# Kernel tuning notes

Measured on AMD Instinct MI355X. Metric: run time of the kernel, lower is better.

Reference implementation:

```python
import jax, jax.numpy as jnp
import numpy as np

DIM = 256
HEADS = 8
HEAD_DIM = 32
WS = 64
MLP = 1024
INNER = HEADS * HEAD_DIM
EPS = 1e-5


def setup_inputs() -> dict:
    key = jax.random.key(0)
    ks = jax.random.split(key, 10)
    B, N = 2, 65536
    s = lambda fan_in: 1.0 / np.sqrt(fan_in)
    return {
        "x": jax.random.normal(ks[0], (B, N, DIM), jnp.float32),
        "w_qkv": jax.random.normal(ks[1], (DIM, 3 * INNER), jnp.float32) * s(DIM),
        "w_out": jax.random.normal(ks[2], (INNER, DIM), jnp.float32) * s(INNER),
        "b_out": jnp.zeros((DIM,), jnp.float32),
        "pos_emb": jax.random.normal(ks[3], (WS, WS), jnp.float32),
        "ln1_g": jnp.ones((DIM,), jnp.float32),
        "ln1_b": jnp.zeros((DIM,), jnp.float32),
        "w1": jax.random.normal(ks[4], (DIM, MLP), jnp.float32) * s(DIM),
        "b1": jnp.zeros((MLP,), jnp.float32),
        "w2": jax.random.normal(ks[5], (MLP, DIM), jnp.float32) * s(MLP),
        "b2": jnp.zeros((DIM,), jnp.float32),
        "ln2_g": jnp.ones((DIM,), jnp.float32),
        "ln2_b": jnp.zeros((DIM,), jnp.float32),
    }


def layernorm(x, g, b):
    mu = jnp.mean(x, axis=-1, keepdims=True)
    var = jnp.var(x, axis=-1, keepdims=True)
    return (x - mu) * jax.lax.rsqrt(var + EPS) * g + b


def window_attn(x, w_qkv, w_out, b_out, pos_emb):
    # shifted window attention (displacement = WS // 2)
    disp = WS // 2
    x = jnp.roll(x, -disp, axis=1)
    b, n, _ = x.shape
    n_w = n // WS
    qkv = x @ w_qkv  # [b, n, 3*inner]
    qkv = qkv.reshape(b, n_w, WS, 3, HEADS, HEAD_DIM)
    q = jnp.transpose(qkv[:, :, :, 0], (0, 3, 1, 2, 4))  # [b, h, n_w, ws, d]
    k = jnp.transpose(qkv[:, :, :, 1], (0, 3, 1, 2, 4))
    v = jnp.transpose(qkv[:, :, :, 2], (0, 3, 1, 2, 4))
    scale = HEAD_DIM ** -0.5
    dots = jnp.einsum("bhwid,bhwjd->bhwij", q, k) * scale + pos_emb
    attn = jax.nn.softmax(dots, axis=-1)
    out = jnp.einsum("bhwij,bhwjd->bhwid", attn, v)
    out = jnp.transpose(out, (0, 2, 3, 1, 4)).reshape(b, n, INNER)
    out = out @ w_out + b_out
    return jnp.roll(out, disp, axis=1)


def reference(x, w_qkv, w_out, b_out, pos_emb, ln1_g, ln1_b, w1, b1, w2, b2, ln2_g, ln2_b):
    # PointSwinBlock: Residual(PreNorm(attn)) then Residual(PreNorm(ffn))
    x = x + window_attn(layernorm(x, ln1_g, ln1_b), w_qkv, w_out, b_out, pos_emb)
    h = layernorm(x, ln2_g, ln2_b)
    h = jax.nn.gelu(h @ w1 + b1, approximate=False) @ w2 + b2
    return x + h
```

## Files before the change

### kernel.cpp

```cpp
#include <hip/hip_runtime.h>
#include <hip/hip_bf16.h>
#include <math.h>
#include <stdint.h>

#define DIM   256
#define NSEQ  65536
#define NTOK  131072
#define HEADS 8
#define HD    32
#define WSZ   64
#define NWIN  2048
#define QKVN  768
#define MLPD  1024
#define LNEPS 1e-5f

typedef __bf16 bf16;
typedef __bf16 bf16x8 __attribute__((ext_vector_type(8)));
typedef __bf16 bf16x4 __attribute__((ext_vector_type(4)));
typedef float  f32x4  __attribute__((ext_vector_type(4)));

__device__ __forceinline__ int roll_row(int r) {
  return (r & 0x10000) | ((r + 32) & 0xFFFF);
}

__device__ __forceinline__ float fast_gelu(float v) {
  const float x2 = v * v;
  const float z2 = v * __builtin_fmaf(x2, 0.07135481630268f, 1.5957691216057308f);
  const float e  = __expf(z2);
  const float r  = __builtin_amdgcn_rcpf(e + 1.0f);
  return __builtin_fmaf(-v, r, v);
}

template<int NY>
__device__ __forceinline__ void grid_swz(int& mBase, int& nBase) {
  const int nwg  = gridDim.x;
  const int lin  = blockIdx.x;
  const int orig = (lin & 7) * (nwg >> 3) + (lin >> 3);
  mBase = (orig / NY) * 128;
  nBase = (orig % NY) * 128;
}

__device__ __forceinline__ void stage16(const bf16* g, bf16* l) {
#if __has_builtin(__builtin_amdgcn_global_load_lds)
  __builtin_amdgcn_global_load_lds((const __attribute__((address_space(1))) void*)g,
                                   (__attribute__((address_space(3))) void*)l, 16, 0, 0);
#else
  int lane = threadIdx.x & 63;
  *(uint4*)((char*)l + lane * 16) = *(const uint4*)g;
#endif
}

template<int K, int LDB, bool ROLL>
__device__ __forceinline__ void gemm_tile(const bf16* __restrict__ A,
                                          const bf16* __restrict__ Bt,
                                          int mBase, int nBase,
                                          bf16* sA, bf16* sB,
                                          f32x4 acc[4][4])
{
  const int tid  = threadIdx.x;
  const int wave = tid >> 6;
  const int lane = tid & 63;
  const int slot = lane & 3;
  const int swz  = (lane >> 3) & 3;
  const int rloc = lane >> 2;
  const int chunk = ((slot ^ swz) * 8);

  int lr0 = mBase + wave * 32 + rloc;
  int lr1 = lr0 + 16;
  int ar0 = ROLL ? roll_row(lr0) : lr0;
  int ar1 = ROLL ? roll_row(lr1) : lr1;
  const bf16* gA0 = A + (size_t)ar0 * K + chunk;
  const bf16* gA1 = A + (size_t)ar1 * K + chunk;
  const bf16* gB0 = Bt + (size_t)(nBase + wave * 32 + rloc) * LDB + chunk;
  const bf16* gB1 = Bt + (size_t)(nBase + wave * 32 + rloc + 16) * LDB + chunk;

  bf16* dA0 = sA + (wave * 32 +  0) * 32;
  bf16* dA1 = sA + (wave * 32 + 16) * 32;
  bf16* dB0 = sB + (wave * 32 +  0) * 32;
  bf16* dB1 = sB + (wave * 32 + 16) * 32;

  const int m0 = (wave & 1) * 64;
  const int n0 = (wave >> 1) * 64;
  const int c    = lane & 15;
  const int quad = lane >> 4;

  int fa[4], fb[4];
#pragma unroll
  for (int t = 0; t < 4; ++t) {
    int rowA = m0 + t * 16 + c;
    fa[t] = rowA * 32 + ((quad ^ ((rowA >> 1) & 3)) * 8);
    int rowB = n0 + t * 16 + c;
    fb[t] = rowB * 32 + ((quad ^ ((rowB >> 1) & 3)) * 8);
  }

  const f32x4 fzero = {0.f, 0.f, 0.f, 0.f};
#pragma unroll
  for (int i = 0; i < 4; ++i)
#pragma unroll
    for (int j = 0; j < 4; ++j) acc[i][j] = fzero;

  stage16(gA0, dA0);
  stage16(gA1, dA1);
  stage16(gB0, dB0);
  stage16(gB1, dB1);
  __syncthreads();

  int cur = 0;
  for (int k0 = 0; k0 < K; k0 += 32) {
    const int nxt = cur ^ 1;
    if (k0 + 32 < K) {
      const int o = nxt * 4096;
      stage16(gA0 + k0 + 32, dA0 + o);
      stage16(gA1 + k0 + 32, dA1 + o);
      stage16(gB0 + k0 + 32, dB0 + o);
      stage16(gB1 + k0 + 32, dB1 + o);
    }
    const int co = cur * 4096;
    bf16x8 afr[4], bfr[4];
#pragma unroll
    for (int t = 0; t < 4; ++t) {
      afr[t] = *(const bf16x8*)(sA + co + fa[t]);
      bfr[t] = *(const bf16x8*)(sB + co + fb[t]);
    }
#pragma unroll
    for (int i = 0; i < 4; ++i)
#pragma unroll
      for (int j = 0; j < 4; ++j)
        acc[i][j] = __builtin_amdgcn_mfma_f32_16x16x32_bf16(afr[i], bfr[j], acc[i][j], 0, 0, 0);
    __syncthreads();
    cur = nxt;
  }
}

__global__ __launch_bounds__(256) void k_prep(const float* __restrict__ wqkv,
                                              const float* __restrict__ wout,
                                              const float* __restrict__ w1,
                                              const float* __restrict__ w2,
                                              const float* __restrict__ pos,
                                              bf16* __restrict__ wqkvT, bf16* __restrict__ woutT,
                                              bf16* __restrict__ w1T, bf16* __restrict__ w2T,
                                              float* __restrict__ posP)
{
  const int total = 768 * 256 + 256 * 256 + 1024 * 256 + 256 * 1024 + 4096;
  for (int i = blockIdx.x * 256 + threadIdx.x; i < total; i += gridDim.x * 256) {
    int j = i;
    if (j < 768 * 256) { int n = j >> 8, k = j & 255; wqkvT[j] = (bf16)wqkv[k * 768 + n]; continue; }
    j -= 768 * 256;
    if (j < 256 * 256) { int n = j >> 8, k = j & 255; woutT[j] = (bf16)wout[k * 256 + n]; continue; }
    j -= 256 * 256;
    if (j < 1024 * 256) { int n = j >> 8, k = j & 255; w1T[j] = (bf16)w1[k * 1024 + n]; continue; }
    j -= 1024 * 256;
    if (j < 256 * 1024) { int n = j >> 10, k = j & 1023; w2T[j] = (bf16)w2[k * 256 + n]; continue; }
    j -= 256 * 1024;
    {
      int lane = j & 63, t = j >> 6;
      int nt = t & 3, r = (t >> 2) & 3, mt = t >> 4;
      int ii = mt * 16 + (lane >> 4) * 4 + r, jj = nt * 16 + (lane & 15);
      posP[j] = pos[ii * 64 + jj];
    }
  }
}

__global__ __launch_bounds__(256) void k_ln(const float* __restrict__ x,
                                            const float* __restrict__ gam,
                                            const float* __restrict__ bet,
                                            bf16* __restrict__ out)
{
  const int wave = threadIdx.x >> 6, lane = threadIdx.x & 63;
  const int token = blockIdx.x * 4 + wave;
  const float4 v = ((const float4*)x)[(size_t)token * 64 + lane];
  float s = v.x + v.y + v.z + v.w;
  float q = v.x * v.x + v.y * v.y + v.z * v.z + v.w * v.w;
#pragma unroll
  for (int off = 32; off; off >>= 1) { s += __shfl_xor(s, off); q += __shfl_xor(q, off); }
  const float mu = s * (1.f / 256.f);
  const float var = q * (1.f / 256.f) - mu * mu;
  const float rs = rsqrtf(var + LNEPS);
  const float4 gv = ((const float4*)gam)[lane];
  const float4 bv = ((const float4*)bet)[lane];
  bf16x4 o;
  o[0] = (bf16)((v.x - mu) * rs * gv.x + bv.x);
  o[1] = (bf16)((v.y - mu) * rs * gv.y + bv.y);
  o[2] = (bf16)((v.z - mu) * rs * gv.z + bv.z);
  o[3] = (bf16)((v.w - mu) * rs * gv.w + bv.w);
  *(bf16x4*)(out + (size_t)token * 256 + lane * 4) = o;
}

__global__ __launch_bounds__(256, 2) void k_gemm_qkv(const bf16* __restrict__ h1,
                                                     const bf16* __restrict__ wqkvT,
                                                     bf16* __restrict__ qkv)
{
  __shared__ __align__(16) bf16 sA[2 * 128 * 32];
  __shared__ __align__(16) bf16 sB[2 * 128 * 32];
  f32x4 acc[4][4];
  int mBase, nBase;
  grid_swz<6>(mBase, nBase);
  gemm_tile<256, 256, true>(h1, wqkvT, mBase, nBase, sA, sB, acc);
  const int lane = threadIdx.x & 63, wave = threadIdx.x >> 6;
  const int c = lane & 15, quad = lane >> 4;
  const int rowBase = mBase + (wave & 1) * 64 + quad * 4;
  const int colBase = nBase + (wave >> 1) * 64 + c;
#pragma unroll
  for (int i = 0; i < 4; ++i)
#pragma unroll
    for (int j = 0; j < 4; ++j)
#pragma unroll
      for (int r = 0; r < 4; ++r)
        qkv[(size_t)(rowBase + i * 16 + r) * QKVN + (colBase + j * 16)] = (bf16)acc[i][j][r];
}

__global__ __launch_bounds__(256, 2) void k_attn(const bf16* __restrict__ qkv,
                                                 const float* __restrict__ posP,
                                                 bf16* __restrict__ attn)
{
  __shared__ __align__(16) bf16 sQ[4][64 * 40];
  __shared__ __align__(16) bf16 sK[4][64 * 40];
  __shared__ __align__(16) bf16 sV[4][32 * 72];
  const int tid = threadIdx.x;
  const int wave = tid >> 6, lane = tid & 63;
  const int gh = blockIdx.y * 4 + wave;
  const int win = blockIdx.x;
  const int c = lane & 15, quad = lane >> 4;
  const size_t base = (size_t)win * 64 * QKVN;

  {
    const int row = lane >> 2;
    const int col = (lane & 3) * 8;
#pragma unroll
    for (int i = 0; i < 4; ++i) {
      int rr = i * 16 + row;
      *(uint4*)(&sQ[wave][rr * 40 + col]) = *(const uint4*)(qkv + base + (size_t)rr * QKVN + gh * 32 + col);
      *(uint4*)(&sK[wave][rr * 40 + col]) = *(const uint4*)(qkv + base + (size_t)rr * QKVN + 256 + gh * 32 + col);
    }
  }
  {
    const int d = lane & 31, jh = lane >> 5;
#pragma unroll
    for (int it = 0; it < 32; ++it) {
      int j = it * 2 + jh;
      sV[wave][d * 72 + j] = qkv[base + (size_t)j * QKVN + 512 + gh * 32 + d];
    }
  }

  const f32x4 fzero = {0.f, 0.f, 0.f, 0.f};
  f32x4 sacc[4][4];
#pragma unroll
  for (int i = 0; i < 4; ++i)
#pragma unroll
    for (int j = 0; j < 4; ++j) sacc[i][j] = fzero;
  bf16x8 qf[4], kf[4];
#pragma unroll
  for (int t = 0; t < 4; ++t) {
    qf[t] = *(const bf16x8*)(&sQ[wave][(t * 16 + c) * 40 + quad * 8]);
    kf[t] = *(const bf16x8*)(&sK[wave][(t * 16 + c) * 40 + quad * 8]);
  }
#pragma unroll
  for (int i = 0; i < 4; ++i)
#pragma unroll
    for (int j = 0; j < 4; ++j)
      sacc[i][j] = __builtin_amdgcn_mfma_f32_16x16x32_bf16(qf[i], kf[j], sacc[i][j], 0, 0, 0);

  const float scale = 0.17677669529663687f;
  float p[4][4][4];
#pragma unroll
  for (int i = 0; i < 4; ++i)
#pragma unroll
    for (int j = 0; j < 4; ++j)
#pragma unroll
      for (int r = 0; r < 4; ++r)
        p[i][j][r] = sacc[i][j][r] * scale + posP[(((i * 4 + r) * 4 + j) << 6) + lane];

  float mx[4][4], rcp[4][4];
#pragma unroll
  for (int i = 0; i < 4; ++i)
#pragma unroll
    for (int r = 0; r < 4; ++r) {
      float m = fmaxf(fmaxf(p[i][0][r], p[i][1][r]), fmaxf(p[i][2][r], p[i][3][r]));
      m = fmaxf(m, __shfl_xor(m, 1)); m = fmaxf(m, __shfl_xor(m, 2));
      m = fmaxf(m, __shfl_xor(m, 4)); m = fmaxf(m, __shfl_xor(m, 8));
      mx[i][r] = m;
    }
#pragma unroll
  for (int i = 0; i < 4; ++i)
#pragma unroll
    for (int r = 0; r < 4; ++r) {
#pragma unroll
      for (int j = 0; j < 4; ++j) p[i][j][r] = __expf(p[i][j][r] - mx[i][r]);
      float t = p[i][0][r] + p[i][1][r] + p[i][2][r] + p[i][3][r];
      t += __shfl_xor(t, 1); t += __shfl_xor(t, 2); t += __shfl_xor(t, 4); t += __shfl_xor(t, 8);
      rcp[i][r] = 1.0f / t;
    }
#pragma unroll
  for (int i = 0; i < 4; ++i)
#pragma unroll
    for (int j = 0; j < 4; ++j)
#pragma unroll
      for (int r = 0; r < 4; ++r) p[i][j][r] *= rcp[i][r];

  f32x4 oacc[4][2];
#pragma unroll
  for (int i = 0; i < 4; ++i) { oacc[i][0] = fzero; oacc[i][1] = fzero; }
#pragma unroll
  for (int half = 0; half < 2; ++half) {
#pragma unroll
    for (int i = 0; i < 4; ++i)
#pragma unroll
      for (int j2 = 0; j2 < 2; ++j2)
#pragma unroll
        for (int r = 0; r < 4; ++r)
          sQ[wave][(i * 16 + quad * 4 + r) * 40 + j2 * 16 + c] = (bf16)p[i][half * 2 + j2][r];
    bf16x8 pf[4], vf[2];
#pragma unroll
    for (int t = 0; t < 4; ++t)
      pf[t] = *(const bf16x8*)(&sQ[wave][(t * 16 + c) * 40 + quad * 8]);
#pragma unroll
    for (int n2 = 0; n2 < 2; ++n2)
      vf[n2] = *(const bf16x8*)(&sV[wave][(n2 * 16 + c) * 72 + half * 32 + quad * 8]);
#pragma unroll
    for (int i = 0; i < 4; ++i)
#pragma unroll
      for (int n2 = 0; n2 < 2; ++n2)
        oacc[i][n2] = __builtin_amdgcn_mfma_f32_16x16x32_bf16(pf[i], vf[n2], oacc[i][n2], 0, 0, 0);
  }

#pragma unroll
  for (int i = 0; i < 4; ++i)
#pragma unroll
    for (int n2 = 0; n2 < 2; ++n2)
#pragma unroll
      for (int r = 0; r < 4; ++r)
        attn[(size_t)(win * 64 + i * 16 + quad * 4 + r) * DIM + gh * 32 + n2 * 16 + c] = (bf16)oacc[i][n2][r];
}

__global__ __launch_bounds__(256, 2) void k_gemm_proj(const bf16* __restrict__ attn,
                                                      const bf16* __restrict__ woutT,
                                                      const float* __restrict__ x,
                                                      const float* __restrict__ b_out,
                                                      float* __restrict__ x2)
{
  __shared__ __align__(16) bf16 sA[2 * 128 * 32];
  __shared__ __align__(16) bf16 sB[2 * 128 * 32];
  f32x4 acc[4][4];
  int mBase, nBase;
  grid_swz<2>(mBase, nBase);
  gemm_tile<256, 256, false>(attn, woutT, mBase, nBase, sA, sB, acc);
  const int lane = threadIdx.x & 63, wave = threadIdx.x >> 6;
  const int c = lane & 15, quad = lane >> 4;
  const int rowBase = mBase + (wave & 1) * 64 + quad * 4;
  const int colBase = nBase + (wave >> 1) * 64 + c;
#pragma unroll
  for (int i = 0; i < 4; ++i)
#pragma unroll
    for (int r = 0; r < 4; ++r) {
      const int rp = rowBase + i * 16 + r;
      const size_t rowoff = (size_t)roll_row(rp) * DIM;
#pragma unroll
      for (int j = 0; j < 4; ++j) {
        const int col = colBase + j * 16;
        x2[rowoff + col] = acc[i][j][r] + b_out[col] + x[rowoff + col];
      }
    }
}

template<int LDC, int NY>
__global__ __launch_bounds__(256, 2) void k_gemm_mlp1(const bf16* __restrict__ h2,
                                                      const bf16* __restrict__ w1Th,
                                                      const float* __restrict__ b1h,
                                                      bf16* __restrict__ g)
{
  __shared__ __align__(16) bf16 sA[2 * 128 * 32];
  __shared__ __align__(16) bf16 sB[2 * 128 * 32];
  f32x4 acc[4][4];
  int mBase, nBase;
  grid_swz<NY>(mBase, nBase);
  gemm_tile<256, 256, false>(h2, w1Th, mBase, nBase, sA, sB, acc);
  const int lane = threadIdx.x & 63, wave = threadIdx.x >> 6;
  const int c = lane & 15, quad = lane >> 4;
  const int rowBase = mBase + (wave & 1) * 64 + quad * 4;
  const int colBase = nBase + (wave >> 1) * 64 + c;
#pragma unroll
  for (int i = 0; i < 4; ++i)
#pragma unroll
    for (int j = 0; j < 4; ++j) {
      const int col = colBase + j * 16;
      const float bb = b1h[col];
#pragma unroll
      for (int r = 0; r < 4; ++r) {
        const float v = acc[i][j][r] + bb;
        g[(size_t)(rowBase + i * 16 + r) * LDC + col] = (bf16)fast_gelu(v);
      }
    }
}

template<int K>
__global__ __launch_bounds__(256, 2) void k_gemm_mlp2(const bf16* __restrict__ g,
                                                      const bf16* __restrict__ w2Th,
                                                      const float* __restrict__ b2,
                                                      float* __restrict__ out,
                                                      int first)
{
  __shared__ __align__(16) bf16 sA[2 * 128 * 32];
  __shared__ __align__(16) bf16 sB[2 * 128 * 32];
  f32x4 acc[4][4];
  int mBase, nBase;
  grid_swz<2>(mBase, nBase);
  gemm_tile<K, 1024, false>(g, w2Th, mBase, nBase, sA, sB, acc);
  const int lane = threadIdx.x & 63, wave = threadIdx.x >> 6;
  const int c = lane & 15, quad = lane >> 4;
  const int rowBase = mBase + (wave & 1) * 64 + quad * 4;
  const int colBase = nBase + (wave >> 1) * 64 + c;
#pragma unroll
  for (int i = 0; i < 4; ++i)
#pragma unroll
    for (int j = 0; j < 4; ++j) {
      const int col = colBase + j * 16;
      const float bb = first ? b2[col] : 0.0f;
#pragma unroll
      for (int r = 0; r < 4; ++r) {
        const size_t off = (size_t)(rowBase + i * 16 + r) * DIM + col;
        out[off] = out[off] + acc[i][j][r] + bb;
      }
    }
}

extern "C" void kernel_launch(void* const* d_in, const int* in_sizes, int n_in,
                              void* d_out, int out_size, void* d_ws, size_t ws_size,
                              hipStream_t stream) {
  const float* x    = (const float*)d_in[0];
  const float* wqkv = (const float*)d_in[1];
  const float* wout = (const float*)d_in[2];
  const float* bo   = (const float*)d_in[3];
  const float* pos  = (const float*)d_in[4];
  const float* l1g  = (const float*)d_in[5];
  const float* l1b  = (const float*)d_in[6];
  const float* w1   = (const float*)d_in[7];
  const float* b1   = (const float*)d_in[8];
  const float* w2   = (const float*)d_in[9];
  const float* b2   = (const float*)d_in[10];
  const float* l2g  = (const float*)d_in[11];
  const float* l2b  = (const float*)d_in[12];
  float* out = (float*)d_out;

  char* ws = (char*)d_ws;
  const size_t WEIGHTS_SZ = (size_t)768 * 256 * 2 + 256 * 256 * 2 + 1024 * 256 * 2
                          + 256 * 1024 * 2 + 4096 * 4;
  const size_t FUSED_NEED = 67108864ull + 268435456ull + WEIGHTS_SZ;
  const bool fused = ws_size >= FUSED_NEED;

  bf16* h1   = (bf16*)ws;
  bf16* qkv  = (bf16*)(ws + 67108864);
  bf16* attn = h1;
  bf16* h2;
  bf16* gbuf;
  char* wp;
  if (fused) {
    h2   = (bf16*)ws;
    gbuf = (bf16*)(ws + 67108864);
    wp   = ws + 67108864 + 268435456;
  } else {
    h2   = qkv;
    gbuf = (bf16*)(ws + 134217728);
    wp   = ws + 268435456;
  }
  bf16* wqkvT = (bf16*)wp;  wp += 768 * 256 * 2;
  bf16* woutT = (bf16*)wp;  wp += 256 * 256 * 2;
  bf16* w1T   = (bf16*)wp;  wp += 1024 * 256 * 2;
  bf16* w2T   = (bf16*)wp;  wp += 256 * 1024 * 2;
  float* posP = (float*)wp;

  k_prep<<<dim3(1024), dim3(256), 0, stream>>>(wqkv, wout, w1, w2, pos, wqkvT, woutT, w1T, w2T, posP);
  k_ln<<<dim3(NTOK / 4), dim3(256), 0, stream>>>(x, l1g, l1b, h1);
  k_gemm_qkv<<<dim3(6144), dim3(256), 0, stream>>>(h1, wqkvT, qkv);
  k_attn<<<dim3(NWIN, 2), dim3(256), 0, stream>>>(qkv, posP, attn);
  k_gemm_proj<<<dim3(2048), dim3(256), 0, stream>>>(attn, woutT, x, bo, out);
  k_ln<<<dim3(NTOK / 4), dim3(256), 0, stream>>>(out, l2g, l2b, h2);
  if (fused) {
    k_gemm_mlp1<1024, 8><<<dim3(8192), dim3(256), 0, stream>>>(h2, w1T, b1, gbuf);
    k_gemm_mlp2<1024><<<dim3(2048), dim3(256), 0, stream>>>(gbuf, w2T, b2, out, 1);
  } else {
    for (int half = 0; half < 2; ++half) {
      k_gemm_mlp1<512, 4><<<dim3(4096), dim3(256), 0, stream>>>(h2, w1T + half * 512 * 256, b1 + half * 512, gbuf);
      k_gemm_mlp2<512><<<dim3(2048), dim3(256), 0, stream>>>(gbuf, w2T + half * 512, b2, out, half == 0 ? 1 : 0);
    }
  }
}
```

Measured before the change: 797.5 us.

## Triple-buffer GEMM LDS staging with partial vmcnt waits and split barriers

Replaces the double-buffered K loop in the shared GEMM tile with a three-stage ring buffer that keeps two async global-to-LDS loads in flight. Each stage waits only for the oldest load using partial vmcnt counts and raw s_barrier instead of a full __syncthreads. Fragment reads are followed by an lgkmcnt wait and a barrier before the MFMAs, so the next overwrite is safe. The goal is to hide more global load latency. The cost is 50% more LDS per block, which could reduce occupancy under the 2-blocks-per-CU launch bound.

```diff
diff --git a/kernel.cpp b/kernel.cpp
--- a/kernel.cpp
+++ b/kernel.cpp
@@ -50,6 +50,28 @@
 #endif
 }
 
+#define TILE_ELEMS 4096
+
+__device__ __forceinline__ void gemm_step(const bf16* sA, const bf16* sB, int co,
+                                          const int fa[4], const int fb[4],
+                                          f32x4 acc[4][4])
+{
+  bf16x8 afr[4], bfr[4];
+#pragma unroll
+  for (int t = 0; t < 4; ++t) {
+    afr[t] = *(const bf16x8*)(sA + co + fa[t]);
+    bfr[t] = *(const bf16x8*)(sB + co + fb[t]);
+  }
+  asm volatile("s_waitcnt lgkmcnt(0)" ::: "memory");
+  __builtin_amdgcn_s_barrier();
+  __builtin_amdgcn_sched_barrier(0);
+#pragma unroll
+  for (int i = 0; i < 4; ++i)
+#pragma unroll
+    for (int j = 0; j < 4; ++j)
+      acc[i][j] = __builtin_amdgcn_mfma_f32_16x16x32_bf16(afr[i], bfr[j], acc[i][j], 0, 0, 0);
+}
+
 template<int K, int LDB, bool ROLL>
 __device__ __forceinline__ void gemm_tile(const bf16* __restrict__ A,
                                           const bf16* __restrict__ Bt,
@@ -99,37 +121,42 @@
 #pragma unroll
     for (int j = 0; j < 4; ++j) acc[i][j] = fzero;
 
+  constexpr int NT = K / 32;
+  static_assert(NT >= 3, "need at least 3 k-chunks");
+
   stage16(gA0, dA0);
   stage16(gA1, dA1);
   stage16(gB0, dB0);
   stage16(gB1, dB1);
-  __syncthreads();
+  stage16(gA0 + 32, dA0 + TILE_ELEMS);
+  stage16(gA1 + 32, dA1 + TILE_ELEMS);
+  stage16(gB0 + 32, dB0 + TILE_ELEMS);
+  stage16(gB1 + 32, dB1 + TILE_ELEMS);
 
   int cur = 0;
-  for (int k0 = 0; k0 < K; k0 += 32) {
-    const int nxt = cur ^ 1;
-    if (k0 + 32 < K) {
-      const int o = nxt * 4096;
-      stage16(gA0 + k0 + 32, dA0 + o);
-      stage16(gA1 + k0 + 32, dA1 + o);
-      stage16(gB0 + k0 + 32, dB0 + o);
-      stage16(gB1 + k0 + 32, dB1 + o);
-    }
-    const int co = cur * 4096;
-    bf16x8 afr[4], bfr[4];
-#pragma unroll
-    for (int t = 0; t < 4; ++t) {
-      afr[t] = *(const bf16x8*)(sA + co + fa[t]);
-      bfr[t] = *(const bf16x8*)(sB + co + fb[t]);
-    }
-#pragma unroll
-    for (int i = 0; i < 4; ++i)
-#pragma unroll
-      for (int j = 0; j < 4; ++j)
-        acc[i][j] = __builtin_amdgcn_mfma_f32_16x16x32_bf16(afr[i], bfr[j], acc[i][j], 0, 0, 0);
-    __syncthreads();
-    cur = nxt;
-  }
+  for (int t = 0; t < NT - 2; ++t) {
+    const int nxt2 = (cur == 0) ? 2 : cur - 1;
+    const int o = nxt2 * TILE_ELEMS;
+    const int k2 = (t + 2) * 32;
+    stage16(gA0 + k2, dA0 + o);
+    stage16(gA1 + k2, dA1 + o);
+    stage16(gB0 + k2, dB0 + o);
+    stage16(gB1 + k2, dB1 + o);
+    asm volatile("s_waitcnt vmcnt(8)" ::: "memory");
+    __builtin_amdgcn_s_barrier();
+    __builtin_amdgcn_sched_barrier(0);
+    gemm_step(sA, sB, cur * TILE_ELEMS, fa, fb, acc);
+    cur = (cur == 2) ? 0 : cur + 1;
+  }
+  asm volatile("s_waitcnt vmcnt(4)" ::: "memory");
+  __builtin_amdgcn_s_barrier();
+  __builtin_amdgcn_sched_barrier(0);
+  gemm_step(sA, sB, cur * TILE_ELEMS, fa, fb, acc);
+  cur = (cur == 2) ? 0 : cur + 1;
+  asm volatile("s_waitcnt vmcnt(0)" ::: "memory");
+  __builtin_amdgcn_s_barrier();
+  __builtin_amdgcn_sched_barrier(0);
+  gemm_step(sA, sB, cur * TILE_ELEMS, fa, fb, acc);
 }
 
 __global__ __launch_bounds__(256) void k_prep(const float* __restrict__ wqkv,
@@ -190,8 +217,8 @@
                                                      const bf16* __restrict__ wqkvT,
                                                      bf16* __restrict__ qkv)
 {
-  __shared__ __align__(16) bf16 sA[2 * 128 * 32];
-  __shared__ __align__(16) bf16 sB[2 * 128 * 32];
+  __shared__ __align__(16) bf16 sA[3 * TILE_ELEMS];
+  __shared__ __align__(16) bf16 sB[3 * TILE_ELEMS];
   f32x4 acc[4][4];
   int mBase, nBase;
   grid_swz<6>(mBase, nBase);
@@ -338,8 +365,8 @@
                                                       const float* __restrict__ b_out,
                                                       float* __restrict__ x2)
 {
-  __shared__ __align__(16) bf16 sA[2 * 128 * 32];
-  __shared__ __align__(16) bf16 sB[2 * 128 * 32];
+  __shared__ __align__(16) bf16 sA[3 * TILE_ELEMS];
+  __shared__ __align__(16) bf16 sB[3 * TILE_ELEMS];
   f32x4 acc[4][4];
   int mBase, nBase;
   grid_swz<2>(mBase, nBase);
@@ -368,8 +395,8 @@
                                                       const float* __restrict__ b1h,
                                                       bf16* __restrict__ g)
 {
-  __shared__ __align__(16) bf16 sA[2 * 128 * 32];
-  __shared__ __align__(16) bf16 sB[2 * 128 * 32];
+  __shared__ __align__(16) bf16 sA[3 * TILE_ELEMS];
+  __shared__ __align__(16) bf16 sB[3 * TILE_ELEMS];
   f32x4 acc[4][4];
   int mBase, nBase;
   grid_swz<NY>(mBase, nBase);
@@ -399,8 +426,8 @@
                                                       float* __restrict__ out,
                                                       int first)
 {
-  __shared__ __align__(16) bf16 sA[2 * 128 * 32];
-  __shared__ __align__(16) bf16 sB[2 * 128 * 32];
+  __shared__ __align__(16) bf16 sA[3 * TILE_ELEMS];
+  __shared__ __align__(16) bf16 sB[3 * TILE_ELEMS];
   f32x4 acc[4][4];
   int mBase, nBase;
   grid_swz<2>(mBase, nBase);
```

Result: no change. 797.1 us (-0.0%).

## Fuse layernorm into QKV GEMM and fuse whole MLP into one kernel

Applied to the files above, without the earlier changes.

Merges LN1 (including the roll) into the QKV projection kernel and LN2, MLP1, GELU and MLP2 into a single per-64-row kernel. The 1024-wide GELU intermediate now stays in LDS in 128-column chunks instead of going through global memory, and the separate normalized-activation buffers are gone. B fragments are read straight from global memory without LDS staging, and the MLP kernel syncs twice per chunk, which may limit MFMA throughput.

```diff
diff --git a/kernel.cpp b/kernel.cpp
--- a/kernel.cpp
+++ b/kernel.cpp
@@ -161,14 +161,9 @@
   }
 }
 
-__global__ __launch_bounds__(256) void k_ln(const float* __restrict__ x,
-                                            const float* __restrict__ gam,
-                                            const float* __restrict__ bet,
-                                            bf16* __restrict__ out)
-{
-  const int wave = threadIdx.x >> 6, lane = threadIdx.x & 63;
-  const int token = blockIdx.x * 4 + wave;
-  const float4 v = ((const float4*)x)[(size_t)token * 64 + lane];
+__device__ __forceinline__ void ln_row_to_lds(const float4 v, const float4 gv, const float4 bv,
+                                              int r, bf16* sA, int lane)
+{
   float s = v.x + v.y + v.z + v.w;
   float q = v.x * v.x + v.y * v.y + v.z * v.z + v.w * v.w;
 #pragma unroll
@@ -176,37 +171,181 @@
   const float mu = s * (1.f / 256.f);
   const float var = q * (1.f / 256.f) - mu * mu;
   const float rs = rsqrtf(var + LNEPS);
-  const float4 gv = ((const float4*)gam)[lane];
-  const float4 bv = ((const float4*)bet)[lane];
   bf16x4 o;
   o[0] = (bf16)((v.x - mu) * rs * gv.x + bv.x);
   o[1] = (bf16)((v.y - mu) * rs * gv.y + bv.y);
   o[2] = (bf16)((v.z - mu) * rs * gv.z + bv.z);
   o[3] = (bf16)((v.w - mu) * rs * gv.w + bv.w);
-  *(bf16x4*)(out + (size_t)token * 256 + lane * 4) = o;
-}
-
-__global__ __launch_bounds__(256, 2) void k_gemm_qkv(const bf16* __restrict__ h1,
-                                                     const bf16* __restrict__ wqkvT,
-                                                     bf16* __restrict__ qkv)
-{
-  __shared__ __align__(16) bf16 sA[2 * 128 * 32];
-  __shared__ __align__(16) bf16 sB[2 * 128 * 32];
-  f32x4 acc[4][4];
-  int mBase, nBase;
-  grid_swz<6>(mBase, nBase);
-  gemm_tile<256, 256, true>(h1, wqkvT, mBase, nBase, sA, sB, acc);
-  const int lane = threadIdx.x & 63, wave = threadIdx.x >> 6;
+  const int q8  = lane >> 3;
+  const int oct = (lane >> 1) & 3;
+  const int w   = (r >> 1) & 3;
+  *(bf16x4*)(sA + q8 * 2048 + r * 32 + ((oct ^ w) * 8) + (lane & 1) * 4) = o;
+}
+
+__global__ __launch_bounds__(512) void k_qkvln(const float* __restrict__ x,
+                                               const float* __restrict__ gam,
+                                               const float* __restrict__ bet,
+                                               const bf16* __restrict__ wqkvT,
+                                               bf16* __restrict__ qkv)
+{
+  __shared__ __align__(16) bf16 sA[8 * 64 * 32];
+  const int tid  = threadIdx.x;
+  const int wave = tid >> 6, lane = tid & 63;
+  const int lin  = blockIdx.x;
+  const int blk  = (lin & 7) * (gridDim.x >> 3) + (lin >> 3);
+  const int m0   = blk * 64;
+
+  {
+    const float4 gv = ((const float4*)gam)[lane];
+    const float4 bv = ((const float4*)bet)[lane];
+#pragma unroll
+    for (int t = 0; t < 8; ++t) {
+      const int r = wave * 8 + t;
+      const float4 v = ((const float4*)x)[(size_t)roll_row(m0 + r) * 64 + lane];
+      ln_row_to_lds(v, gv, bv, r, sA, lane);
+    }
+  }
+  __syncthreads();
+
   const int c = lane & 15, quad = lane >> 4;
-  const int rowBase = mBase + (wave & 1) * 64 + quad * 4;
-  const int colBase = nBase + (wave >> 1) * 64 + c;
-#pragma unroll
-  for (int i = 0; i < 4; ++i)
-#pragma unroll
-    for (int j = 0; j < 4; ++j)
+  int fa[4];
+#pragma unroll
+  for (int t = 0; t < 4; ++t) {
+    int rowA = t * 16 + c;
+    fa[t] = rowA * 32 + ((quad ^ ((rowA >> 1) & 3)) * 8);
+  }
+
+  const f32x4 fzero = {0.f, 0.f, 0.f, 0.f};
+  f32x4 acc[4][6];
+#pragma unroll
+  for (int i = 0; i < 4; ++i)
+#pragma unroll
+    for (int bn = 0; bn < 6; ++bn) acc[i][bn] = fzero;
+
+  const bf16* bp = wqkvT + (size_t)(wave * 96 + c) * 256 + quad * 8;
+#pragma unroll
+  for (int ks = 0; ks < 8; ++ks) {
+    bf16x8 a[4];
+#pragma unroll
+    for (int t = 0; t < 4; ++t) a[t] = *(const bf16x8*)(sA + ks * 2048 + fa[t]);
+    bf16x8 b[6];
+#pragma unroll
+    for (int bn = 0; bn < 6; ++bn) b[bn] = *(const bf16x8*)(bp + (size_t)bn * 16 * 256 + ks * 32);
+#pragma unroll
+    for (int i = 0; i < 4; ++i)
+#pragma unroll
+      for (int bn = 0; bn < 6; ++bn)
+        acc[i][bn] = __builtin_amdgcn_mfma_f32_16x16x32_bf16(a[i], b[bn], acc[i][bn], 0, 0, 0);
+  }
+
+#pragma unroll
+  for (int i = 0; i < 4; ++i)
+#pragma unroll
+    for (int bn = 0; bn < 6; ++bn)
 #pragma unroll
       for (int r = 0; r < 4; ++r)
-        qkv[(size_t)(rowBase + i * 16 + r) * QKVN + (colBase + j * 16)] = (bf16)acc[i][j][r];
+        qkv[(size_t)(m0 + i * 16 + quad * 4 + r) * QKVN + (wave * 96 + bn * 16 + c)] = (bf16)acc[i][bn][r];
+}
+
+__global__ __launch_bounds__(512) void k_mlp(const float* __restrict__ gam,
+                                             const float* __restrict__ bet,
+                                             const bf16* __restrict__ w1T,
+                                             const float* __restrict__ b1,
+                                             const bf16* __restrict__ w2T,
+                                             const float* __restrict__ b2,
+                                             float* out)
+{
+  __shared__ __align__(16) bf16 sA[8 * 64 * 32];
+  __shared__ __align__(16) bf16 sP[4 * 64 * 32];
+  const int tid  = threadIdx.x;
+  const int wave = tid >> 6, lane = tid & 63;
+  const int lin  = blockIdx.x;
+  const int blk  = (lin & 7) * (gridDim.x >> 3) + (lin >> 3);
+  const int m0   = blk * 64;
+
+  {
+    const float4 gv = ((const float4*)gam)[lane];
+    const float4 bv = ((const float4*)bet)[lane];
+#pragma unroll
+    for (int t = 0; t < 8; ++t) {
+      const int r = wave * 8 + t;
+      const float4 v = ((const float4*)out)[(size_t)(m0 + r) * 64 + lane];
+      ln_row_to_lds(v, gv, bv, r, sA, lane);
+    }
+  }
+  __syncthreads();
+
+  const int c = lane & 15, quad = lane >> 4;
+  int fa[4];
+#pragma unroll
+  for (int t = 0; t < 4; ++t) {
+    int rowA = t * 16 + c;
+    fa[t] = rowA * 32 + ((quad ^ ((rowA >> 1) & 3)) * 8);
+  }
+
+  const f32x4 fzero = {0.f, 0.f, 0.f, 0.f};
+  f32x4 acc2[4][2];
+#pragma unroll
+  for (int i = 0; i < 4; ++i) { acc2[i][0] = fzero; acc2[i][1] = fzero; }
+
+  const int nq  = wave >> 1;
+  const int oct = ((wave & 1) << 1) | (c >> 3);
+  const int ncl = c & 7;
+
+  for (int ch = 0; ch < 8; ++ch) {
+    f32x4 acc1[4];
+#pragma unroll
+    for (int i = 0; i < 4; ++i) acc1[i] = fzero;
+    const bf16* bp1 = w1T + (size_t)(ch * 128 + wave * 16 + c) * 256 + quad * 8;
+#pragma unroll
+    for (int ks = 0; ks < 8; ++ks) {
+      bf16x8 a[4];
+#pragma unroll
+      for (int t = 0; t < 4; ++t) a[t] = *(const bf16x8*)(sA + ks * 2048 + fa[t]);
+      const bf16x8 b = *(const bf16x8*)(bp1 + ks * 32);
+#pragma unroll
+      for (int i = 0; i < 4; ++i)
+        acc1[i] = __builtin_amdgcn_mfma_f32_16x16x32_bf16(a[i], b, acc1[i], 0, 0, 0);
+    }
+    __syncthreads();
+    const float bb = b1[ch * 128 + wave * 16 + c];
+#pragma unroll
+    for (int i = 0; i < 4; ++i)
+#pragma unroll
+      for (int r = 0; r < 4; ++r) {
+        const int m = i * 16 + quad * 4 + r;
+        const int w = (m >> 1) & 3;
+        sP[nq * 2048 + m * 32 + ((oct ^ w) * 8) + ncl] = (bf16)fast_gelu(acc1[i][r] + bb);
+      }
+    __syncthreads();
+    const bf16* bp2 = w2T + (size_t)(wave * 32 + c) * 1024 + ch * 128 + quad * 8;
+#pragma unroll
+    for (int ks = 0; ks < 4; ++ks) {
+      bf16x8 pa[4];
+#pragma unroll
+      for (int t = 0; t < 4; ++t) pa[t] = *(const bf16x8*)(sP + ks * 2048 + fa[t]);
+      const bf16x8 b0 = *(const bf16x8*)(bp2 + ks * 32);
+      const bf16x8 b1f = *(const bf16x8*)(bp2 + (size_t)16 * 1024 + ks * 32);
+#pragma unroll
+      for (int i = 0; i < 4; ++i) {
+        acc2[i][0] = __builtin_amdgcn_mfma_f32_16x16x32_bf16(pa[i], b0, acc2[i][0], 0, 0, 0);
+        acc2[i][1] = __builtin_amdgcn_mfma_f32_16x16x32_bf16(pa[i], b1f, acc2[i][1], 0, 0, 0);
+      }
+    }
+  }
+
+#pragma unroll
+  for (int j = 0; j < 2; ++j) {
+    const int col = wave * 32 + j * 16 + c;
+    const float bb2 = b2[col];
+#pragma unroll
+    for (int i = 0; i < 4; ++i)
+#pragma unroll
+      for (int r = 0; r < 4; ++r) {
+        const size_t off = (size_t)(m0 + i * 16 + quad * 4 + r) * DIM + col;
+        out[off] = out[off] + acc2[i][j][r] + bb2;
+      }
+  }
 }
 
 __global__ __launch_bounds__(256, 2) void k_attn(const bf16* __restrict__ qkv,
@@ -338,8 +477,8 @@
                                                       const float* __restrict__ b_out,
                                                       float* __restrict__ x2)
 {
-  __shared__ __align__(16) bf16 sA[2 * 128 * 32];
-  __shared__ __align__(16) bf16 sB[2 * 128 * 32];
+  __shared__ __align__(16) bf16 sA[2 * 4096];
+  __shared__ __align__(16) bf16 sB[2 * 4096];
   f32x4 acc[4][4];
   int mBase, nBase;
   grid_swz<2>(mBase, nBase);
@@ -358,67 +497,6 @@
       for (int j = 0; j < 4; ++j) {
         const int col = colBase + j * 16;
         x2[rowoff + col] = acc[i][j][r] + b_out[col] + x[rowoff + col];
-      }
-    }
-}
-
-template<int LDC, int NY>
-__global__ __launch_bounds__(256, 2) void k_gemm_mlp1(const bf16* __restrict__ h2,
-                                                      const bf16* __restrict__ w1Th,
-                                                      const float* __restrict__ b1h,
-                                                      bf16* __restrict__ g)
-{
-  __shared__ __align__(16) bf16 sA[2 * 128 * 32];
-  __shared__ __align__(16) bf16 sB[2 * 128 * 32];
-  f32x4 acc[4][4];
-  int mBase, nBase;
-  grid_swz<NY>(mBase, nBase);
-  gemm_tile<256, 256, false>(h2, w1Th, mBase, nBase, sA, sB, acc);
-  const int lane = threadIdx.x & 63, wave = threadIdx.x >> 6;
-  const int c = lane & 15, quad = lane >> 4;
-  const int rowBase = mBase + (wave & 1) * 64 + quad * 4;
-  const int colBase = nBase + (wave >> 1) * 64 + c;
-#pragma unroll
-  for (int i = 0; i < 4; ++i)
-#pragma unroll
-    for (int j = 0; j < 4; ++j) {
-      const int col = colBase + j * 16;
-      const float bb = b1h[col];
-#pragma unroll
-      for (int r = 0; r < 4; ++r) {
-        const float v = acc[i][j][r] + bb;
-        g[(size_t)(rowBase + i * 16 + r) * LDC + col] = (bf16)fast_gelu(v);
-      }
-    }
-}
-
-template<int K>
-__global__ __launch_bounds__(256, 2) void k_gemm_mlp2(const bf16* __restrict__ g,
-                                                      const bf16* __restrict__ w2Th,
-                                                      const float* __restrict__ b2,
-                                                      float* __restrict__ out,
-                                                      int first)
-{
-  __shared__ __align__(16) bf16 sA[2 * 128 * 32];
-  __shared__ __align__(16) bf16 sB[2 * 128 * 32];
-  f32x4 acc[4][4];
-  int mBase, nBase;
-  grid_swz<2>(mBase, nBase);
-  gemm_tile<K, 1024, false>(g, w2Th, mBase, nBase, sA, sB, acc);
-  const int lane = threadIdx.x & 63, wave = threadIdx.x >> 6;
-  const int c = lane & 15, quad = lane >> 4;
-  const int rowBase = mBase + (wave & 1) * 64 + quad * 4;
-  const int colBase = nBase + (wave >> 1) * 64 + c;
-#pragma unroll
-  for (int i = 0; i < 4; ++i)
-#pragma unroll
-    for (int j = 0; j < 4; ++j) {
-      const int col = colBase + j * 16;
-      const float bb = first ? b2[col] : 0.0f;
-#pragma unroll
-      for (int r = 0; r < 4; ++r) {
-        const size_t off = (size_t)(rowBase + i * 16 + r) * DIM + col;
-        out[off] = out[off] + acc[i][j][r] + bb;
       }
     }
 }
@@ -442,26 +520,9 @@
   float* out = (float*)d_out;
 
   char* ws = (char*)d_ws;
-  const size_t WEIGHTS_SZ = (size_t)768 * 256 * 2 + 256 * 256 * 2 + 1024 * 256 * 2
-                          + 256 * 1024 * 2 + 4096 * 4;
-  const size_t FUSED_NEED = 67108864ull + 268435456ull + WEIGHTS_SZ;
-  const bool fused = ws_size >= FUSED_NEED;
-
-  bf16* h1   = (bf16*)ws;
-  bf16* qkv  = (bf16*)(ws + 67108864);
-  bf16* attn = h1;
-  bf16* h2;
-  bf16* gbuf;
-  char* wp;
-  if (fused) {
-    h2   = (bf16*)ws;
-    gbuf = (bf16*)(ws + 67108864);
-    wp   = ws + 67108864 + 268435456;
-  } else {
-    h2   = qkv;
-    gbuf = (bf16*)(ws + 134217728);
-    wp   = ws + 268435456;
-  }
+  bf16* qkv  = (bf16*)ws;
+  bf16* attn = (bf16*)(ws + 201326592);
+  char* wp   = ws + 268435456;
   bf16* wqkvT = (bf16*)wp;  wp += 768 * 256 * 2;
   bf16* woutT = (bf16*)wp;  wp += 256 * 256 * 2;
   bf16* w1T   = (bf16*)wp;  wp += 1024 * 256 * 2;
@@ -469,18 +530,8 @@
   float* posP = (float*)wp;
 
   k_prep<<<dim3(1024), dim3(256), 0, stream>>>(wqkv, wout, w1, w2, pos, wqkvT, woutT, w1T, w2T, posP);
-  k_ln<<<dim3(NTOK / 4), dim3(256), 0, stream>>>(x, l1g, l1b, h1);
-  k_gemm_qkv<<<dim3(6144), dim3(256), 0, stream>>>(h1, wqkvT, qkv);
+  k_qkvln<<<dim3(NTOK / 64), dim3(512), 0, stream>>>(x, l1g, l1b, wqkvT, qkv);
   k_attn<<<dim3(NWIN, 2), dim3(256), 0, stream>>>(qkv, posP, attn);
   k_gemm_proj<<<dim3(2048), dim3(256), 0, stream>>>(attn, woutT, x, bo, out);
-  k_ln<<<dim3(NTOK / 4), dim3(256), 0, stream>>>(out, l2g, l2b, h2);
-  if (fused) {
-    k_gemm_mlp1<1024, 8><<<dim3(8192), dim3(256), 0, stream>>>(h2, w1T, b1, gbuf);
-    k_gemm_mlp2<1024><<<dim3(2048), dim3(256), 0, stream>>>(gbuf, w2T, b2, out, 1);
-  } else {
-    for (int half = 0; half < 2; ++half) {
-      k_gemm_mlp1<512, 4><<<dim3(4096), dim3(256), 0, stream>>>(h2, w1T + half * 512 * 256, b1 + half * 512, gbuf);
-      k_gemm_mlp2<512><<<dim3(2048), dim3(256), 0, stream>>>(gbuf, w2T + half * 512, b2, out, half == 0 ? 1 : 0);
-    }
-  }
-}
+  k_mlp<<<dim3(NTOK / 64), dim3(512), 0, stream>>>(l2g, l2b, w1T, b1, w2T, b2, out);
+}
```

Result: slower. 844.8 us (+5.9%).

## Fuse window attention with output projection and residual add into one kernel

Applied to the files above, without the earlier changes.

Window attention and the output projection GEMM now run in one kernel per window. Each block processes all 8 heads for its window, keeps the 64x256 attention output in shared memory, and multiplies it by the projection weight read from global memory. It then adds bias and residual with the roll applied. This removes the bf16 attention intermediate write/read and one launch, and Q/K fragments are now loaded straight from global memory instead of staged through LDS. The cost is a serial loop over heads, half as many blocks, projection weights loaded per block without LDS staging, and more shared memory per block.

```diff
diff --git a/kernel.cpp b/kernel.cpp
--- a/kernel.cpp
+++ b/kernel.cpp
@@ -190,8 +190,8 @@
                                                      const bf16* __restrict__ wqkvT,
                                                      bf16* __restrict__ qkv)
 {
-  __shared__ __align__(16) bf16 sA[2 * 128 * 32];
-  __shared__ __align__(16) bf16 sB[2 * 128 * 32];
+  __shared__ __align__(16) bf16 sA[2 * 4096];
+  __shared__ __align__(16) bf16 sB[2 * 4096];
   f32x4 acc[4][4];
   int mBase, nBase;
   grid_swz<6>(mBase, nBase);
@@ -209,155 +209,159 @@
         qkv[(size_t)(rowBase + i * 16 + r) * QKVN + (colBase + j * 16)] = (bf16)acc[i][j][r];
 }
 
-__global__ __launch_bounds__(256, 2) void k_attn(const bf16* __restrict__ qkv,
-                                                 const float* __restrict__ posP,
-                                                 bf16* __restrict__ attn)
-{
-  __shared__ __align__(16) bf16 sQ[4][64 * 40];
-  __shared__ __align__(16) bf16 sK[4][64 * 40];
+__global__ __launch_bounds__(256, 2) void k_attnproj(const bf16* __restrict__ qkv,
+                                                     const float* __restrict__ posP,
+                                                     const bf16* __restrict__ woutT,
+                                                     const float* __restrict__ x,
+                                                     const float* __restrict__ b_out,
+                                                     float* __restrict__ out)
+{
   __shared__ __align__(16) bf16 sV[4][32 * 72];
+  __shared__ __align__(16) bf16 sP[4][64 * 40];
+  __shared__ __align__(16) bf16 sO[64 * 264];
   const int tid = threadIdx.x;
   const int wave = tid >> 6, lane = tid & 63;
-  const int gh = blockIdx.y * 4 + wave;
   const int win = blockIdx.x;
   const int c = lane & 15, quad = lane >> 4;
   const size_t base = (size_t)win * 64 * QKVN;
-
-  {
-    const int row = lane >> 2;
-    const int col = (lane & 3) * 8;
-#pragma unroll
-    for (int i = 0; i < 4; ++i) {
-      int rr = i * 16 + row;
-      *(uint4*)(&sQ[wave][rr * 40 + col]) = *(const uint4*)(qkv + base + (size_t)rr * QKVN + gh * 32 + col);
-      *(uint4*)(&sK[wave][rr * 40 + col]) = *(const uint4*)(qkv + base + (size_t)rr * QKVN + 256 + gh * 32 + col);
-    }
-  }
-  {
-    const int d = lane & 31, jh = lane >> 5;
-#pragma unroll
-    for (int it = 0; it < 32; ++it) {
-      int j = it * 2 + jh;
-      sV[wave][d * 72 + j] = qkv[base + (size_t)j * QKVN + 512 + gh * 32 + d];
-    }
-  }
-
   const f32x4 fzero = {0.f, 0.f, 0.f, 0.f};
-  f32x4 sacc[4][4];
-#pragma unroll
-  for (int i = 0; i < 4; ++i)
-#pragma unroll
-    for (int j = 0; j < 4; ++j) sacc[i][j] = fzero;
-  bf16x8 qf[4], kf[4];
-#pragma unroll
-  for (int t = 0; t < 4; ++t) {
-    qf[t] = *(const bf16x8*)(&sQ[wave][(t * 16 + c) * 40 + quad * 8]);
-    kf[t] = *(const bf16x8*)(&sK[wave][(t * 16 + c) * 40 + quad * 8]);
-  }
-#pragma unroll
-  for (int i = 0; i < 4; ++i)
+  const float scale = 0.17677669529663687f;
+
+  for (int hh = 0; hh < 2; ++hh) {
+    const int gh = hh * 4 + wave;
+
+    {
+      const int d = lane & 31, jh = lane >> 5;
+#pragma unroll
+      for (int it = 0; it < 32; ++it) {
+        int j = it * 2 + jh;
+        sV[wave][d * 72 + j] = qkv[base + (size_t)j * QKVN + 512 + gh * 32 + d];
+      }
+    }
+
+    bf16x8 qf[4], kf[4];
+#pragma unroll
+    for (int t = 0; t < 4; ++t) {
+      qf[t] = *(const bf16x8*)(qkv + base + (size_t)(t * 16 + c) * QKVN + gh * 32 + quad * 8);
+      kf[t] = *(const bf16x8*)(qkv + base + (size_t)(t * 16 + c) * QKVN + 256 + gh * 32 + quad * 8);
+    }
+
+    f32x4 sacc[4][4];
+#pragma unroll
+    for (int i = 0; i < 4; ++i)
+#pragma unroll
+      for (int j = 0; j < 4; ++j) sacc[i][j] = fzero;
+#pragma unroll
+    for (int i = 0; i < 4; ++i)
+#pragma unroll
+      for (int j = 0; j < 4; ++j)
+        sacc[i][j] = __builtin_amdgcn_mfma_f32_16x16x32_bf16(qf[i], kf[j], sacc[i][j], 0, 0, 0);
+
+    float p[4][4][4];
+#pragma unroll
+    for (int i = 0; i < 4; ++i)
+#pragma unroll
+      for (int j = 0; j < 4; ++j)
+#pragma unroll
+        for (int r = 0; r < 4; ++r)
+          p[i][j][r] = sacc[i][j][r] * scale + posP[(((i * 4 + r) * 4 + j) << 6) + lane];
+
+    float mx[4][4], rcp[4][4];
+#pragma unroll
+    for (int i = 0; i < 4; ++i)
+#pragma unroll
+      for (int r = 0; r < 4; ++r) {
+        float m = fmaxf(fmaxf(p[i][0][r], p[i][1][r]), fmaxf(p[i][2][r], p[i][3][r]));
+        m = fmaxf(m, __shfl_xor(m, 1)); m = fmaxf(m, __shfl_xor(m, 2));
+        m = fmaxf(m, __shfl_xor(m, 4)); m = fmaxf(m, __shfl_xor(m, 8));
+        mx[i][r] = m;
+      }
+#pragma unroll
+    for (int i = 0; i < 4; ++i)
+#pragma unroll
+      for (int r = 0; r < 4; ++r) {
+#pragma unroll
+        for (int j = 0; j < 4; ++j) p[i][j][r] = __expf(p[i][j][r] - mx[i][r]);
+        float t = p[i][0][r] + p[i][1][r] + p[i][2][r] + p[i][3][r];
+        t += __shfl_xor(t, 1); t += __shfl_xor(t, 2); t += __shfl_xor(t, 4); t += __shfl_xor(t, 8);
+        rcp[i][r] = 1.0f / t;
+      }
+#pragma unroll
+    for (int i = 0; i < 4; ++i)
+#pragma unroll
+      for (int j = 0; j < 4; ++j)
+#pragma unroll
+        for (int r = 0; r < 4; ++r) p[i][j][r] *= rcp[i][r];
+
+    f32x4 oacc[4][2];
+#pragma unroll
+    for (int i = 0; i < 4; ++i) { oacc[i][0] = fzero; oacc[i][1] = fzero; }
+#pragma unroll
+    for (int half = 0; half < 2; ++half) {
+#pragma unroll
+      for (int i = 0; i < 4; ++i)
+#pragma unroll
+        for (int j2 = 0; j2 < 2; ++j2)
+#pragma unroll
+          for (int r = 0; r < 4; ++r)
+            sP[wave][(i * 16 + quad * 4 + r) * 40 + j2 * 16 + c] = (bf16)p[i][half * 2 + j2][r];
+      bf16x8 pf[4], vf[2];
+#pragma unroll
+      for (int t = 0; t < 4; ++t)
+        pf[t] = *(const bf16x8*)(&sP[wave][(t * 16 + c) * 40 + quad * 8]);
+#pragma unroll
+      for (int n2 = 0; n2 < 2; ++n2)
+        vf[n2] = *(const bf16x8*)(&sV[wave][(n2 * 16 + c) * 72 + half * 32 + quad * 8]);
+#pragma unroll
+      for (int i = 0; i < 4; ++i)
+#pragma unroll
+        for (int n2 = 0; n2 < 2; ++n2)
+          oacc[i][n2] = __builtin_amdgcn_mfma_f32_16x16x32_bf16(pf[i], vf[n2], oacc[i][n2], 0, 0, 0);
+    }
+
+#pragma unroll
+    for (int i = 0; i < 4; ++i)
+#pragma unroll
+      for (int n2 = 0; n2 < 2; ++n2)
+#pragma unroll
+        for (int r = 0; r < 4; ++r)
+          sO[(i * 16 + quad * 4 + r) * 264 + gh * 32 + n2 * 16 + c] = (bf16)oacc[i][n2][r];
+  }
+
+  __syncthreads();
+
+  f32x4 acc[4][4];
+#pragma unroll
+  for (int i = 0; i < 4; ++i)
+#pragma unroll
+    for (int j = 0; j < 4; ++j) acc[i][j] = fzero;
+
+#pragma unroll
+  for (int ks = 0; ks < 8; ++ks) {
+    bf16x8 a[4], b[4];
+#pragma unroll
+    for (int t = 0; t < 4; ++t)
+      a[t] = *(const bf16x8*)(&sO[(t * 16 + c) * 264 + ks * 32 + quad * 8]);
 #pragma unroll
     for (int j = 0; j < 4; ++j)
-      sacc[i][j] = __builtin_amdgcn_mfma_f32_16x16x32_bf16(qf[i], kf[j], sacc[i][j], 0, 0, 0);
-
-  const float scale = 0.17677669529663687f;
-  float p[4][4][4];
-#pragma unroll
-  for (int i = 0; i < 4; ++i)
-#pragma unroll
-    for (int j = 0; j < 4; ++j)
-#pragma unroll
-      for (int r = 0; r < 4; ++r)
-        p[i][j][r] = sacc[i][j][r] * scale + posP[(((i * 4 + r) * 4 + j) << 6) + lane];
-
-  float mx[4][4], rcp[4][4];
+      b[j] = *(const bf16x8*)(woutT + (size_t)(wave * 64 + j * 16 + c) * 256 + ks * 32 + quad * 8);
+#pragma unroll
+    for (int i = 0; i < 4; ++i)
+#pragma unroll
+      for (int j = 0; j < 4; ++j)
+        acc[i][j] = __builtin_amdgcn_mfma_f32_16x16x32_bf16(a[i], b[j], acc[i][j], 0, 0, 0);
+  }
+
 #pragma unroll
   for (int i = 0; i < 4; ++i)
 #pragma unroll
     for (int r = 0; r < 4; ++r) {
-      float m = fmaxf(fmaxf(p[i][0][r], p[i][1][r]), fmaxf(p[i][2][r], p[i][3][r]));
-      m = fmaxf(m, __shfl_xor(m, 1)); m = fmaxf(m, __shfl_xor(m, 2));
-      m = fmaxf(m, __shfl_xor(m, 4)); m = fmaxf(m, __shfl_xor(m, 8));
-      mx[i][r] = m;
-    }
-#pragma unroll
-  for (int i = 0; i < 4; ++i)
-#pragma unroll
-    for (int r = 0; r < 4; ++r) {
-#pragma unroll
-      for (int j = 0; j < 4; ++j) p[i][j][r] = __expf(p[i][j][r] - mx[i][r]);
-      float t = p[i][0][r] + p[i][1][r] + p[i][2][r] + p[i][3][r];
-      t += __shfl_xor(t, 1); t += __shfl_xor(t, 2); t += __shfl_xor(t, 4); t += __shfl_xor(t, 8);
-      rcp[i][r] = 1.0f / t;
-    }
-#pragma unroll
-  for (int i = 0; i < 4; ++i)
-#pragma unroll
-    for (int j = 0; j < 4; ++j)
-#pragma unroll
-      for (int r = 0; r < 4; ++r) p[i][j][r] *= rcp[i][r];
-
-  f32x4 oacc[4][2];
-#pragma unroll
-  for (int i = 0; i < 4; ++i) { oacc[i][0] = fzero; oacc[i][1] = fzero; }
-#pragma unroll
-  for (int half = 0; half < 2; ++half) {
-#pragma unroll
-    for (int i = 0; i < 4; ++i)
-#pragma unroll
-      for (int j2 = 0; j2 < 2; ++j2)
-#pragma unroll
-        for (int r = 0; r < 4; ++r)
-          sQ[wave][(i * 16 + quad * 4 + r) * 40 + j2 * 16 + c] = (bf16)p[i][half * 2 + j2][r];
-    bf16x8 pf[4], vf[2];
-#pragma unroll
-    for (int t = 0; t < 4; ++t)
-      pf[t] = *(const bf16x8*)(&sQ[wave][(t * 16 + c) * 40 + quad * 8]);
-#pragma unroll
-    for (int n2 = 0; n2 < 2; ++n2)
-      vf[n2] = *(const bf16x8*)(&sV[wave][(n2 * 16 + c) * 72 + half * 32 + quad * 8]);
-#pragma unroll
-    for (int i = 0; i < 4; ++i)
-#pragma unroll
-      for (int n2 = 0; n2 < 2; ++n2)
-        oacc[i][n2] = __builtin_amdgcn_mfma_f32_16x16x32_bf16(pf[i], vf[n2], oacc[i][n2], 0, 0, 0);
-  }
-
-#pragma unroll
-  for (int i = 0; i < 4; ++i)
-#pragma unroll
-    for (int n2 = 0; n2 < 2; ++n2)
-#pragma unroll
-      for (int r = 0; r < 4; ++r)
-        attn[(size_t)(win * 64 + i * 16 + quad * 4 + r) * DIM + gh * 32 + n2 * 16 + c] = (bf16)oacc[i][n2][r];
-}
-
-__global__ __launch_bounds__(256, 2) void k_gemm_proj(const bf16* __restrict__ attn,
-                                                      const bf16* __restrict__ woutT,
-                                                      const float* __restrict__ x,
-                                                      const float* __restrict__ b_out,
-                                                      float* __restrict__ x2)
-{
-  __shared__ __align__(16) bf16 sA[2 * 128 * 32];
-  __shared__ __align__(16) bf16 sB[2 * 128 * 32];
-  f32x4 acc[4][4];
-  int mBase, nBase;
-  grid_swz<2>(mBase, nBase);
-  gemm_tile<256, 256, false>(attn, woutT, mBase, nBase, sA, sB, acc);
-  const int lane = threadIdx.x & 63, wave = threadIdx.x >> 6;
-  const int c = lane & 15, quad = lane >> 4;
-  const int rowBase = mBase + (wave & 1) * 64 + quad * 4;
-  const int colBase = nBase + (wave >> 1) * 64 + c;
-#pragma unroll
-  for (int i = 0; i < 4; ++i)
-#pragma unroll
-    for (int r = 0; r < 4; ++r) {
-      const int rp = rowBase + i * 16 + r;
+      const int rp = win * 64 + i * 16 + quad * 4 + r;
       const size_t rowoff = (size_t)roll_row(rp) * DIM;
 #pragma unroll
       for (int j = 0; j < 4; ++j) {
-        const int col = colBase + j * 16;
-        x2[rowoff + col] = acc[i][j][r] + b_out[col] + x[rowoff + col];
+        const int col = wave * 64 + j * 16 + c;
+        out[rowoff + col] = acc[i][j][r] + b_out[col] + x[rowoff + col];
       }
     }
 }
@@ -368,8 +372,8 @@
                                                       const float* __restrict__ b1h,
                                                       bf16* __restrict__ g)
 {
-  __shared__ __align__(16) bf16 sA[2 * 128 * 32];
-  __shared__ __align__(16) bf16 sB[2 * 128 * 32];
+  __shared__ __align__(16) bf16 sA[2 * 4096];
+  __shared__ __align__(16) bf16 sB[2 * 4096];
   f32x4 acc[4][4];
   int mBase, nBase;
   grid_swz<NY>(mBase, nBase);
@@ -399,8 +403,8 @@
                                                       float* __restrict__ out,
                                                       int first)
 {
-  __shared__ __align__(16) bf16 sA[2 * 128 * 32];
-  __shared__ __align__(16) bf16 sB[2 * 128 * 32];
+  __shared__ __align__(16) bf16 sA[2 * 4096];
+  __shared__ __align__(16) bf16 sB[2 * 4096];
   f32x4 acc[4][4];
   int mBase, nBase;
   grid_swz<2>(mBase, nBase);
@@ -449,7 +453,6 @@
 
   bf16* h1   = (bf16*)ws;
   bf16* qkv  = (bf16*)(ws + 67108864);
-  bf16* attn = h1;
   bf16* h2;
   bf16* gbuf;
   char* wp;
@@ -471,8 +474,7 @@
   k_prep<<<dim3(1024), dim3(256), 0, stream>>>(wqkv, wout, w1, w2, pos, wqkvT, woutT, w1T, w2T, posP);
   k_ln<<<dim3(NTOK / 4), dim3(256), 0, stream>>>(x, l1g, l1b, h1);
   k_gemm_qkv<<<dim3(6144), dim3(256), 0, stream>>>(h1, wqkvT, qkv);
-  k_attn<<<dim3(NWIN, 2), dim3(256), 0, stream>>>(qkv, posP, attn);
-  k_gemm_proj<<<dim3(2048), dim3(256), 0, stream>>>(attn, woutT, x, bo, out);
+  k_attnproj<<<dim3(NWIN), dim3(256), 0, stream>>>(qkv, posP, woutT, x, bo, out);
   k_ln<<<dim3(NTOK / 4), dim3(256), 0, stream>>>(out, l2g, l2b, h2);
   if (fused) {
     k_gemm_mlp1<1024, 8><<<dim3(8192), dim3(256), 0, stream>>>(h2, w1T, b1, gbuf);
```

Result: slower. 888.6 us (+11.4%).
